# Performance work log

Hardware: AMD Instinct MI355X
Metric: run time of the kernel (lower is better)

## Reference

```python
import jax, jax.numpy as jnp
import numpy as np

INPUT_SIZE = 1024
HIDDEN_SIZE = 1024
N_LAYERS = 2
OUTPUT_SIZE = 4096
BATCH = 4096


def setup_inputs() -> dict:
    key = jax.random.key(0)
    ks = jax.random.split(key, 12)
    s = 1.0 / np.sqrt(HIDDEN_SIZE)
    u = lambda k, shp: jax.random.uniform(k, shp, jnp.float32, -s, s)
    return {
        "input": jax.random.normal(ks[0], (1, BATCH, INPUT_SIZE), jnp.float32),
        "hidden": jax.random.normal(ks[1], (N_LAYERS, BATCH, HIDDEN_SIZE), jnp.float32),
        # nn.RNN layer 0 params
        "W_ih0": u(ks[2], (HIDDEN_SIZE, INPUT_SIZE)),
        "W_hh0": u(ks[3], (HIDDEN_SIZE, HIDDEN_SIZE)),
        "b_ih0": u(ks[4], (HIDDEN_SIZE,)),
        "b_hh0": u(ks[5], (HIDDEN_SIZE,)),
        # nn.RNN layer 1 params (input is layer-0 hidden)
        "W_ih1": u(ks[6], (HIDDEN_SIZE, HIDDEN_SIZE)),
        "W_hh1": u(ks[7], (HIDDEN_SIZE, HIDDEN_SIZE)),
        "b_ih1": u(ks[8], (HIDDEN_SIZE,)),
        "b_hh1": u(ks[9], (HIDDEN_SIZE,)),
        # i2o Linear(input_size + hidden_size, output_size)
        "W_out": u(ks[10], (OUTPUT_SIZE, INPUT_SIZE + HIDDEN_SIZE)),
        "b_out": u(ks[11], (OUTPUT_SIZE,)),
    }


def reference(input, hidden, W_ih0, W_hh0, b_ih0, b_hh0,
              W_ih1, W_hh1, b_ih1, b_hh1, W_out, b_out):
    x = input[0]  # [B, input_size] (seq_len == 1)
    # nn.RNN single step, tanh nonlinearity, 2 layers
    h0 = jnp.tanh(x @ W_ih0.T + b_ih0 + hidden[0] @ W_hh0.T + b_hh0)   # [B, H]
    h1 = jnp.tanh(h0 @ W_ih1.T + b_ih1 + hidden[1] @ W_hh1.T + b_hh1)  # [B, H]
    new_hidden = jnp.stack([h0, h1], axis=0)  # [n_layers, B, H]
    # combined = cat(input[0], hidden[0]) where hidden is the NEW hidden
    combined = jnp.concatenate([x, h0], axis=1)  # [B, input+hidden]
    logits = combined @ W_out.T + b_out          # [B, output_size]
    out = jax.nn.log_softmax(logits, axis=1)
    return (out, new_hidden)
```

## Files before the change

kernel.cpp:

```cpp
#include <hip/hip_runtime.h>
#include <math.h>


typedef __attribute__((ext_vector_type(8))) short bf16x8;
typedef __attribute__((ext_vector_type(4))) float f32x4;

__device__ __forceinline__ unsigned short f2b_rne(float f) {
    unsigned int x = __float_as_uint(f);
    x += 0x7FFF + ((x >> 16) & 1);
    return (unsigned short)(x >> 16);
}

__device__ __forceinline__ void gload_lds16(const void* g, void* l) {
    __builtin_amdgcn_global_load_lds(
        (const __attribute__((address_space(1))) void*)g,
        (__attribute__((address_space(3))) void*)l,
        16, 0, 0);
}

struct CvtSeg { const float* src; unsigned short* dst; unsigned n8; };
struct CvtArgs { CvtSeg seg[7]; };

__global__ __launch_bounds__(256) void f2b_multi(CvtArgs a)
{
    unsigned i = blockIdx.x * 256 + threadIdx.x;
#pragma unroll
    for (int s = 0; s < 7; ++s) {
        if (i < a.seg[s].n8) {
            const float4* src = (const float4*)a.seg[s].src;
            float4 u = src[2 * (size_t)i];
            float4 v = src[2 * (size_t)i + 1];
            unsigned short t[8] = {
                f2b_rne(u.x), f2b_rne(u.y), f2b_rne(u.z), f2b_rne(u.w),
                f2b_rne(v.x), f2b_rne(v.y), f2b_rne(v.z), f2b_rne(v.w)};
            *(uint4*)(a.seg[s].dst + 8 * (size_t)i) = *(const uint4*)t;
            return;
        }
        i -= a.seg[s].n8;
    }
}

struct GemmP {
    const unsigned short *Aa, *Ab; int lda;
    const unsigned short *Wa, *Wb; int ldw;
    const float *ba, *bb;
    float* C; int ldc;
    unsigned short* Cb; int ldcb;
    int nx, nb, do_tanh;
};

template<int BM, int BN>
__device__ __forceinline__ void gemm2p_body(
    const GemmP& p, int bid0, unsigned short* As, unsigned short* Ws, int tid)
{
    constexpr int FM = BM / 32;
    constexpr int FN = BN / 32;
    int bid = (bid0 & 7) * (p.nb >> 3) + (bid0 >> 3);
    const int row0 = (bid / p.nx) * BM;
    const int col0 = (bid % p.nx) * BN;

    const int wid = tid >> 6, lane = tid & 63;
    const int wr = wid >> 1, wc = wid & 1;
    const int fr = lane & 15, fk = lane >> 4;

    f32x4 acc[FM][FN] = {};

    for (int h = 0; h < 2; ++h) {
        const unsigned short* A = h ? p.Ab : p.Aa;
        const unsigned short* W = h ? p.Wb : p.Wa;
        for (int k0 = 0; k0 < 1024; k0 += 32) {
#pragma unroll
            for (int i = 0; i < BM / 64; ++i) {
                int c = i * 256 + wid * 64 + lane;
                int r = c >> 2, ol = c & 3;
                int os = ol ^ ((r >> 1) & 3);
                gload_lds16(A + (size_t)(row0 + r) * p.lda + k0 + os * 8,
                            As + (i * 256 + wid * 64) * 8);
            }
#pragma unroll
            for (int i = 0; i < BN / 64; ++i) {
                int c = i * 256 + wid * 64 + lane;
                int r = c >> 2, ol = c & 3;
                int os = ol ^ ((r >> 1) & 3);
                gload_lds16(W + (size_t)(col0 + r) * p.ldw + k0 + os * 8,
                            Ws + (i * 256 + wid * 64) * 8);
            }
            __syncthreads();

            bf16x8 af[FM], wf[FN];
#pragma unroll
            for (int m = 0; m < FM; ++m) {
                int r = wr * (BM / 2) + m * 16 + fr;
                af[m] = *(const bf16x8*)&As[r * 32 + ((fk ^ ((r >> 1) & 3)) * 8)];
            }
#pragma unroll
            for (int n = 0; n < FN; ++n) {
                int r = wc * (BN / 2) + n * 16 + fr;
                wf[n] = *(const bf16x8*)&Ws[r * 32 + ((fk ^ ((r >> 1) & 3)) * 8)];
            }
#pragma unroll
            for (int m = 0; m < FM; ++m)
#pragma unroll
                for (int n = 0; n < FN; ++n)
                    acc[m][n] = __builtin_amdgcn_mfma_f32_16x16x32_bf16(
                        af[m], wf[n], acc[m][n], 0, 0, 0);
            __syncthreads();
        }
    }

    const bool dot = p.do_tanh != 0;
#pragma unroll
    for (int n = 0; n < FN; ++n) {
        const int col = col0 + wc * (BN / 2) + n * 16 + fr;
        float b = p.ba[col];
        if (p.bb) b += p.bb[col];
#pragma unroll
        for (int m = 0; m < FM; ++m) {
#pragma unroll
            for (int j = 0; j < 4; ++j) {
                const int r = row0 + wr * (BM / 2) + m * 16 + fk * 4 + j;
                float v = acc[m][n][j] + b;
                if (dot) v = tanhf(v);
                p.C[(size_t)r * p.ldc + col] = v;
                if (p.Cb) p.Cb[(size_t)r * p.ldcb + col] = f2b_rne(v);
            }
        }
    }
}

__global__ __launch_bounds__(256) void gemm1_k(GemmP p)
{
    __shared__ __align__(16) unsigned short As[128 * 32];
    __shared__ __align__(16) unsigned short Ws[64 * 32];
    gemm2p_body<128, 64>(p, blockIdx.x, As, Ws, threadIdx.x);
}

__device__ __forceinline__ void logsoftmax_row(float* __restrict__ p, int tid)
{
    const int lane = tid & 63;
    const int wv = tid >> 6;
    __shared__ float redm[4];
    __shared__ float reds[4];

    float v[16];
#pragma unroll
    for (int i = 0; i < 16; ++i) v[i] = p[tid + i * 256];

    float m = v[0];
#pragma unroll
    for (int i = 1; i < 16; ++i) m = fmaxf(m, v[i]);
#pragma unroll
    for (int off = 32; off; off >>= 1) m = fmaxf(m, __shfl_xor(m, off));
    if (lane == 0) redm[wv] = m;
    __syncthreads();
    m = fmaxf(fmaxf(redm[0], redm[1]), fmaxf(redm[2], redm[3]));

    float s = 0.f;
#pragma unroll
    for (int i = 0; i < 16; ++i) s += expf(v[i] - m);
#pragma unroll
    for (int off = 32; off; off >>= 1) s += __shfl_xor(s, off);
    if (lane == 0) reds[wv] = s;
    __syncthreads();
    s = reds[0] + reds[1] + reds[2] + reds[3];

    const float lse = m + logf(s);
#pragma unroll
    for (int i = 0; i < 16; ++i) p[tid + i * 256] = v[i] - lse;
}

__global__ __launch_bounds__(256) void g2sm_k(GemmP p, float* __restrict__ logits)
{
    if (blockIdx.x < 256) {
        __shared__ __align__(16) unsigned short As[128 * 32];
        __shared__ __align__(16) unsigned short Ws[128 * 32];
        gemm2p_body<128, 128>(p, blockIdx.x, As, Ws, threadIdx.x);
    } else {
        logsoftmax_row(logits + (size_t)(blockIdx.x - 256) * 4096, threadIdx.x);
    }
}


__device__ __forceinline__ void stage_half8(
    const unsigned short* __restrict__ src, int ld, int base_rc, int tau, int h,
    unsigned short* lds, int wid, int lane, bool isA)
{
    unsigned short* dst = lds + (tau & 1) * 16384 + h * 8192 + wid * 1024;
    const int k0 = (tau & 15) << 6;
#pragma unroll
    for (int i = 0; i < 2; ++i) {
        int c = wid * 128 + i * 64 + lane;
        int ir = c >> 3, cc = c & 7;
        int grow = isA ? (base_rc + h * 64 + (ir & 63) + ((ir >> 6) << 7))
                       : (base_rc + h * 32 + (ir & 31) + ((ir >> 5) << 6));
        int gk = k0 + (((cc ^ ir) & 7) << 3);
        gload_lds16(src + (size_t)grow * ld + gk, dst + i * 512);
    }
}

__global__ __launch_bounds__(512, 2) void gemm8p(
    const unsigned short* __restrict__ Aa, const unsigned short* __restrict__ Ab,
    const unsigned short* __restrict__ Wa, const unsigned short* __restrict__ Wb,
    int lda, int ldw, const float* __restrict__ bias,
    float* __restrict__ C, int ldc, int nx)
{
    constexpr int NT = 32;
    __shared__ __align__(16) unsigned short As[2 * 2 * 128 * 64];
    __shared__ __align__(16) unsigned short Bs[2 * 2 * 128 * 64];

    int bid = blockIdx.x;
    bid = (bid & 7) * 32 + (bid >> 3);
    const int row0 = (bid / nx) * 256;
    const int col0 = (bid % nx) * 256;

    const int tid = threadIdx.x;
    const int wid = tid >> 6, lane = tid & 63;
    const int wr = wid >> 2, wc = wid & 3;
    const int fr = lane & 15, fk = lane >> 4;
    const int ch0 = fk ^ (fr & 7);
    const int ch1 = ch0 ^ 4;

#define STA8(tau, h) stage_half8(((tau) < 16 ? Aa : Ab), lda, row0, (tau), (h), As, wid, lane, true)
#define STB8(tau, h) stage_half8(((tau) < 16 ? Wa : Wb), ldw, col0, (tau), (h), Bs, wid, lane, false)

    f32x4 acc[2][2][4][2] = {};

    STA8(0, 0); STB8(0, 0); STA8(0, 1); STB8(0, 1); STB8(1, 0); STA8(1, 0);
    asm volatile("s_waitcnt vmcnt(4)" ::: "memory");
    __builtin_amdgcn_s_barrier();

#define PHASE8(QM, QN, ...)                                                   \
    {                                                                         \
        const unsigned short* Ap_ = As + buf * 16384 + (QM) * 8192;           \
        const unsigned short* Bp_ = Bs + buf * 16384 + (QN) * 8192;           \
        bf16x8 af[4][2], wf[2][2];                                            \
        _Pragma("unroll") for (int mf = 0; mf < 4; ++mf) {                    \
            int ia = wr * 64 + mf * 16 + fr;                                  \
            af[mf][0] = *(const bf16x8*)&Ap_[ia * 64 + ch0 * 8];              \
            af[mf][1] = *(const bf16x8*)&Ap_[ia * 64 + ch1 * 8];              \
        }                                                                     \
        _Pragma("unroll") for (int nf = 0; nf < 2; ++nf) {                    \
            int ib = wc * 32 + nf * 16 + fr;                                  \
            wf[nf][0] = *(const bf16x8*)&Bp_[ib * 64 + ch0 * 8];              \
            wf[nf][1] = *(const bf16x8*)&Bp_[ib * 64 + ch1 * 8];              \
        }                                                                     \
        __VA_ARGS__                                                           \
        __builtin_amdgcn_s_barrier();                                         \
        asm volatile("s_waitcnt lgkmcnt(0)" ::: "memory");                    \
        __builtin_amdgcn_s_setprio(1);                                        \
        _Pragma("unroll") for (int mf = 0; mf < 4; ++mf)                      \
            _Pragma("unroll") for (int nf = 0; nf < 2; ++nf) {                \
                acc[QM][QN][mf][nf] = __builtin_amdgcn_mfma_f32_16x16x32_bf16(\
                    af[mf][0], wf[nf][0], acc[QM][QN][mf][nf], 0, 0, 0);      \
                acc[QM][QN][mf][nf] = __builtin_amdgcn_mfma_f32_16x16x32_bf16(\
                    af[mf][1], wf[nf][1], acc[QM][QN][mf][nf], 0, 0, 0);      \
            }                                                                 \
        __builtin_amdgcn_s_setprio(0);                                        \
    }

    for (int t = 0; t < NT; ++t) {
        const int buf = t & 1;
        PHASE8(0, 0, { if (t + 1 < NT) { STA8(t + 1, 1); STB8(t + 1, 1); } })
        __builtin_amdgcn_s_barrier();
        PHASE8(1, 0, {})
        __builtin_amdgcn_s_barrier();
        PHASE8(0, 1, { if (t + 2 < NT) STB8(t + 2, 0); })
        __builtin_amdgcn_s_barrier();
        PHASE8(1, 1, { if (t + 2 < NT) STA8(t + 2, 0); })
        if (t < NT - 1) {
            if (t <= NT - 3) asm volatile("s_waitcnt vmcnt(4)" ::: "memory");
            else             asm volatile("s_waitcnt vmcnt(0)" ::: "memory");
        }
        __builtin_amdgcn_s_barrier();
    }
#undef PHASE8
#undef STA8
#undef STB8

#pragma unroll
    for (int qm = 0; qm < 2; ++qm)
#pragma unroll
        for (int qn = 0; qn < 2; ++qn)
#pragma unroll
            for (int nf = 0; nf < 2; ++nf) {
                const int col = col0 + wc * 64 + qn * 32 + nf * 16 + fr;
                const float bv = bias[col];
#pragma unroll
                for (int mf = 0; mf < 4; ++mf) {
                    const int rowb = row0 + wr * 128 + qm * 64 + mf * 16 + fk * 4;
#pragma unroll
                    for (int j = 0; j < 4; ++j)
                        C[(size_t)(rowb + j) * ldc + col] =
                            acc[qm][qn][mf][nf][j] + bv;
                }
            }
}

extern "C" void kernel_launch(void* const* d_in, const int* in_sizes, int n_in,
                              void* d_out, int out_size, void* d_ws, size_t ws_size,
                              hipStream_t stream)
{
    (void)in_sizes; (void)n_in; (void)out_size; (void)ws_size;

    const float* input  = (const float*)d_in[0];
    const float* hidden = (const float*)d_in[1];
    const float* b_ih0  = (const float*)d_in[4];
    const float* b_hh0  = (const float*)d_in[5];
    const float* b_ih1  = (const float*)d_in[8];
    const float* b_hh1  = (const float*)d_in[9];
    const float* b_out  = (const float*)d_in[11];

    float* out = (float*)d_out;
    float* h0  = out + (size_t)4096 * 4096;
    float* h1  = h0 + (size_t)4096 * 1024;

    unsigned short* xb    = (unsigned short*)d_ws;
    unsigned short* hidb  = xb    + (size_t)4096 * 1024;
    unsigned short* h0b   = hidb  + (size_t)2 * 4096 * 1024;
    unsigned short* Wih0b = h0b   + (size_t)4096 * 1024;
    unsigned short* Whh0b = Wih0b + (size_t)1024 * 1024;
    unsigned short* Wih1b = Whh0b + (size_t)1024 * 1024;
    unsigned short* Whh1b = Wih1b + (size_t)1024 * 1024;
    unsigned short* Woutb = Whh1b + (size_t)1024 * 1024;
    unsigned short* hid0b = hidb;
    unsigned short* hid1b = hidb + (size_t)4096 * 1024;

    CvtArgs ca;
    ca.seg[0] = { input,                 xb,    4096u * 1024 / 8 };
    ca.seg[1] = { hidden,                hidb,  2u * 4096 * 1024 / 8 };
    ca.seg[2] = { (const float*)d_in[2], Wih0b, 1024u * 1024 / 8 };
    ca.seg[3] = { (const float*)d_in[3], Whh0b, 1024u * 1024 / 8 };
    ca.seg[4] = { (const float*)d_in[6], Wih1b, 1024u * 1024 / 8 };
    ca.seg[5] = { (const float*)d_in[7], Whh1b, 1024u * 1024 / 8 };
    ca.seg[6] = { (const float*)d_in[10],Woutb, 4096u * 2048 / 8 };
    hipLaunchKernelGGL(f2b_multi, dim3(12288), dim3(256), 0, stream, ca);

    GemmP p1;
    p1.Aa = xb;    p1.Ab = hid0b; p1.lda = 1024;
    p1.Wa = Wih0b; p1.Wb = Whh0b; p1.ldw = 1024;
    p1.ba = b_ih0; p1.bb = b_hh0;
    p1.C = h0; p1.ldc = 1024; p1.Cb = h0b; p1.ldcb = 1024;
    p1.nx = 16; p1.nb = 512; p1.do_tanh = 1;
    hipLaunchKernelGGL(gemm1_k, dim3(512), dim3(256), 0, stream, p1);

    hipLaunchKernelGGL(gemm8p, dim3(256), dim3(512), 0, stream,
                       xb, h0b, Woutb, Woutb + 1024, 1024, 2048,
                       b_out, out, 4096, 16);

    GemmP p2;
    p2.Aa = h0b;   p2.Ab = hid1b; p2.lda = 1024;
    p2.Wa = Wih1b; p2.Wb = Whh1b; p2.ldw = 1024;
    p2.ba = b_ih1; p2.bb = b_hh1;
    p2.C = h1; p2.ldc = 1024; p2.Cb = nullptr; p2.ldcb = 0;
    p2.nx = 8; p2.nb = 256; p2.do_tanh = 1;
    hipLaunchKernelGGL(g2sm_k, dim3(4352), dim3(256), 0, stream, p2, out);
}
```

Measured before the change: 200.3 us.

## Overlap weight conversion with first GEMM, restage gemm8p loop, coalesce epilogue via LDS

The fp32-to-bf16 conversion is split so only the tensors needed by the first GEMM are converted up front. The rest (hidden[1], layer-1 weights, W_out) are converted by extra blocks launched alongside the layer-0 GEMM, so conversion bandwidth overlaps with that GEMM's compute. The big output GEMM's inner loop is reordered to reuse A/B fragments across quadrant phases and to issue fewer LDS reads. Its epilogue now goes through shared memory to write coalesced float4 rows. The costs are more complex scheduling and barriers and an extra LDS round trip in the epilogue.

```diff
diff --git a/kernel.cpp b/kernel.cpp
--- a/kernel.cpp
+++ b/kernel.cpp
@@ -19,13 +19,12 @@
 }
 
 struct CvtSeg { const float* src; unsigned short* dst; unsigned n8; };
-struct CvtArgs { CvtSeg seg[7]; };
-
-__global__ __launch_bounds__(256) void f2b_multi(CvtArgs a)
-{
-    unsigned i = blockIdx.x * 256 + threadIdx.x;
-#pragma unroll
-    for (int s = 0; s < 7; ++s) {
+struct CvtArgs { CvtSeg seg[4]; };
+
+__device__ __forceinline__ void cvt_do(const CvtArgs& a, unsigned i)
+{
+#pragma unroll
+    for (int s = 0; s < 4; ++s) {
         if (i < a.seg[s].n8) {
             const float4* src = (const float4*)a.seg[s].src;
             float4 u = src[2 * (size_t)i];
@@ -40,6 +39,11 @@
     }
 }
 
+__global__ __launch_bounds__(256) void f2b_multi(CvtArgs a)
+{
+    cvt_do(a, blockIdx.x * 256u + threadIdx.x);
+}
+
 struct GemmP {
     const unsigned short *Aa, *Ab; int lda;
     const unsigned short *Wa, *Wb; int ldw;
@@ -128,11 +132,15 @@
     }
 }
 
-__global__ __launch_bounds__(256) void gemm1_k(GemmP p)
-{
-    __shared__ __align__(16) unsigned short As[128 * 32];
-    __shared__ __align__(16) unsigned short Ws[64 * 32];
-    gemm2p_body<128, 64>(p, blockIdx.x, As, Ws, threadIdx.x);
+__global__ __launch_bounds__(256) void g1cvt_k(GemmP p, CvtArgs ca)
+{
+    if (blockIdx.x < 512) {
+        __shared__ __align__(16) unsigned short As[128 * 32];
+        __shared__ __align__(16) unsigned short Ws[64 * 32];
+        gemm2p_body<128, 64>(p, blockIdx.x, As, Ws, threadIdx.x);
+    } else {
+        cvt_do(ca, (blockIdx.x - 512) * 256u + threadIdx.x);
+    }
 }
 
 __device__ __forceinline__ void logsoftmax_row(float* __restrict__ p, int tid)
@@ -205,8 +213,9 @@
     float* __restrict__ C, int ldc, int nx)
 {
     constexpr int NT = 32;
-    __shared__ __align__(16) unsigned short As[2 * 2 * 128 * 64];
-    __shared__ __align__(16) unsigned short Bs[2 * 2 * 128 * 64];
+    __shared__ __align__(16) unsigned short smem[65536];
+    unsigned short* As = smem;
+    unsigned short* Bs = smem + 32768;
 
     int bid = blockIdx.x;
     bid = (bid & 7) * 32 + (bid >> 3);
@@ -223,77 +232,103 @@
 #define STA8(tau, h) stage_half8(((tau) < 16 ? Aa : Ab), lda, row0, (tau), (h), As, wid, lane, true)
 #define STB8(tau, h) stage_half8(((tau) < 16 ? Wa : Wb), ldw, col0, (tau), (h), Bs, wid, lane, false)
 
+#define LDA(QM) { const unsigned short* Ap_ = Abase + (QM) * 8192;            \
+    _Pragma("unroll") for (int mf = 0; mf < 4; ++mf) {                        \
+        int ia = wr * 64 + mf * 16 + fr;                                      \
+        af[mf][0] = *(const bf16x8*)&Ap_[ia * 64 + ch0 * 8];                  \
+        af[mf][1] = *(const bf16x8*)&Ap_[ia * 64 + ch1 * 8]; } }
+
+#define LDB(QN) { const unsigned short* Bp_ = Bbase + (QN) * 8192;            \
+    _Pragma("unroll") for (int nf = 0; nf < 2; ++nf) {                        \
+        int ib = wc * 32 + nf * 16 + fr;                                      \
+        wf[nf][0] = *(const bf16x8*)&Bp_[ib * 64 + ch0 * 8];                  \
+        wf[nf][1] = *(const bf16x8*)&Bp_[ib * 64 + ch1 * 8]; } }
+
+#define MM(QM, QN, ...) {                                                     \
+    __builtin_amdgcn_s_barrier();                                             \
+    asm volatile("s_waitcnt lgkmcnt(0)" ::: "memory");                        \
+    __builtin_amdgcn_s_setprio(1);                                            \
+    _Pragma("unroll") for (int mf = 0; mf < 4; ++mf)                          \
+    _Pragma("unroll") for (int nf = 0; nf < 2; ++nf) {                        \
+        acc[QM][QN][mf][nf] = __builtin_amdgcn_mfma_f32_16x16x32_bf16(        \
+            af[mf][0], wf[nf][0], acc[QM][QN][mf][nf], 0, 0, 0);              \
+        acc[QM][QN][mf][nf] = __builtin_amdgcn_mfma_f32_16x16x32_bf16(        \
+            af[mf][1], wf[nf][1], acc[QM][QN][mf][nf], 0, 0, 0); }            \
+    __builtin_amdgcn_s_setprio(0);                                            \
+    __VA_ARGS__                                                               \
+    __builtin_amdgcn_s_barrier(); }
+
     f32x4 acc[2][2][4][2] = {};
-
-    STA8(0, 0); STB8(0, 0); STA8(0, 1); STB8(0, 1); STB8(1, 0); STA8(1, 0);
+    bf16x8 af[4][2], wf[2][2];
+
+    STA8(0, 0); STB8(0, 1);
+    STA8(0, 1); STB8(0, 0);
+    STA8(1, 0); STB8(1, 1);
     asm volatile("s_waitcnt vmcnt(4)" ::: "memory");
     __builtin_amdgcn_s_barrier();
 
-#define PHASE8(QM, QN, ...)                                                   \
-    {                                                                         \
-        const unsigned short* Ap_ = As + buf * 16384 + (QM) * 8192;           \
-        const unsigned short* Bp_ = Bs + buf * 16384 + (QN) * 8192;           \
-        bf16x8 af[4][2], wf[2][2];                                            \
-        _Pragma("unroll") for (int mf = 0; mf < 4; ++mf) {                    \
-            int ia = wr * 64 + mf * 16 + fr;                                  \
-            af[mf][0] = *(const bf16x8*)&Ap_[ia * 64 + ch0 * 8];              \
-            af[mf][1] = *(const bf16x8*)&Ap_[ia * 64 + ch1 * 8];              \
-        }                                                                     \
-        _Pragma("unroll") for (int nf = 0; nf < 2; ++nf) {                    \
-            int ib = wc * 32 + nf * 16 + fr;                                  \
-            wf[nf][0] = *(const bf16x8*)&Bp_[ib * 64 + ch0 * 8];              \
-            wf[nf][1] = *(const bf16x8*)&Bp_[ib * 64 + ch1 * 8];              \
-        }                                                                     \
-        __VA_ARGS__                                                           \
-        __builtin_amdgcn_s_barrier();                                         \
-        asm volatile("s_waitcnt lgkmcnt(0)" ::: "memory");                    \
-        __builtin_amdgcn_s_setprio(1);                                        \
-        _Pragma("unroll") for (int mf = 0; mf < 4; ++mf)                      \
-            _Pragma("unroll") for (int nf = 0; nf < 2; ++nf) {                \
-                acc[QM][QN][mf][nf] = __builtin_amdgcn_mfma_f32_16x16x32_bf16(\
-                    af[mf][0], wf[nf][0], acc[QM][QN][mf][nf], 0, 0, 0);      \
-                acc[QM][QN][mf][nf] = __builtin_amdgcn_mfma_f32_16x16x32_bf16(\
-                    af[mf][1], wf[nf][1], acc[QM][QN][mf][nf], 0, 0, 0);      \
-            }                                                                 \
-        __builtin_amdgcn_s_setprio(0);                                        \
-    }
-
     for (int t = 0; t < NT; ++t) {
-        const int buf = t & 1;
-        PHASE8(0, 0, { if (t + 1 < NT) { STA8(t + 1, 1); STB8(t + 1, 1); } })
-        __builtin_amdgcn_s_barrier();
-        PHASE8(1, 0, {})
-        __builtin_amdgcn_s_barrier();
-        PHASE8(0, 1, { if (t + 2 < NT) STB8(t + 2, 0); })
-        __builtin_amdgcn_s_barrier();
-        PHASE8(1, 1, { if (t + 2 < NT) STA8(t + 2, 0); })
-        if (t < NT - 1) {
-            if (t <= NT - 3) asm volatile("s_waitcnt vmcnt(4)" ::: "memory");
-            else             asm volatile("s_waitcnt vmcnt(0)" ::: "memory");
-        }
-        __builtin_amdgcn_s_barrier();
-    }
-#undef PHASE8
+        const unsigned short* Abase = As + (t & 1) * 16384;
+        const unsigned short* Bbase = Bs + (t & 1) * 16384;
+
+        LDA(0); LDB(0);
+        if (t + 1 < NT) { STA8(t + 1, 1); STB8(t + 1, 0); }
+        MM(0, 0, )
+        LDB(1);
+        MM(0, 1, )
+        LDA(1);
+        if (t + 2 < NT) STA8(t + 2, 0);
+        MM(1, 1, )
+        LDB(0);
+        if (t + 2 < NT) STB8(t + 2, 1);
+        if (t + 2 < NT) {
+            MM(1, 0, asm volatile("s_waitcnt vmcnt(4)" ::: "memory");)
+        } else if (t + 1 < NT) {
+            MM(1, 0, asm volatile("s_waitcnt vmcnt(0)" ::: "memory");)
+        } else {
+            MM(1, 0, )
+        }
+    }
+#undef MM
+#undef LDA
+#undef LDB
 #undef STA8
 #undef STB8
 
-#pragma unroll
-    for (int qm = 0; qm < 2; ++qm)
+    float bv[2][2];
+#pragma unroll
+    for (int qn = 0; qn < 2; ++qn)
+#pragma unroll
+        for (int nf = 0; nf < 2; ++nf)
+            bv[qn][nf] = bias[col0 + wc * 64 + qn * 32 + nf * 16 + fr];
+
+    float* Ct = (float*)smem;
+#pragma unroll
+    for (int qm = 0; qm < 2; ++qm) {
+        __syncthreads();
 #pragma unroll
         for (int qn = 0; qn < 2; ++qn)
 #pragma unroll
             for (int nf = 0; nf < 2; ++nf) {
-                const int col = col0 + wc * 64 + qn * 32 + nf * 16 + fr;
-                const float bv = bias[col];
-#pragma unroll
-                for (int mf = 0; mf < 4; ++mf) {
-                    const int rowb = row0 + wr * 128 + qm * 64 + mf * 16 + fk * 4;
-#pragma unroll
-                    for (int j = 0; j < 4; ++j)
-                        C[(size_t)(rowb + j) * ldc + col] =
-                            acc[qm][qn][mf][nf][j] + bv;
-                }
-            }
+                const int col = wc * 64 + qn * 32 + nf * 16 + fr;
+#pragma unroll
+                for (int mf = 0; mf < 4; ++mf)
+#pragma unroll
+                    for (int j = 0; j < 4; ++j) {
+                        int lr = wr * 64 + mf * 16 + fk * 4 + j;
+                        Ct[lr * 256 + col] = acc[qm][qn][mf][nf][j] + bv[qn][nf];
+                    }
+            }
+        __syncthreads();
+#pragma unroll
+        for (int k = 0; k < 16; ++k) {
+            int idx = k * 512 + tid;
+            int lrow = idx >> 6, c4 = idx & 63;
+            int grow = row0 + qm * 64 + (lrow & 63) + ((lrow >> 6) << 7);
+            *(float4*)&C[(size_t)grow * ldc + col0 + c4 * 4] =
+                *(const float4*)&Ct[lrow * 256 + c4 * 4];
+        }
+    }
 }
 
 extern "C" void kernel_launch(void* const* d_in, const int* in_sizes, int n_in,
@@ -325,15 +360,12 @@
     unsigned short* hid0b = hidb;
     unsigned short* hid1b = hidb + (size_t)4096 * 1024;
 
-    CvtArgs ca;
-    ca.seg[0] = { input,                 xb,    4096u * 1024 / 8 };
-    ca.seg[1] = { hidden,                hidb,  2u * 4096 * 1024 / 8 };
-    ca.seg[2] = { (const float*)d_in[2], Wih0b, 1024u * 1024 / 8 };
-    ca.seg[3] = { (const float*)d_in[3], Whh0b, 1024u * 1024 / 8 };
-    ca.seg[4] = { (const float*)d_in[6], Wih1b, 1024u * 1024 / 8 };
-    ca.seg[5] = { (const float*)d_in[7], Whh1b, 1024u * 1024 / 8 };
-    ca.seg[6] = { (const float*)d_in[10],Woutb, 4096u * 2048 / 8 };
-    hipLaunchKernelGGL(f2b_multi, dim3(12288), dim3(256), 0, stream, ca);
+    CvtArgs ca1;
+    ca1.seg[0] = { input,                 xb,    524288u };
+    ca1.seg[1] = { hidden,                hidb,  524288u };
+    ca1.seg[2] = { (const float*)d_in[2], Wih0b, 131072u };
+    ca1.seg[3] = { (const float*)d_in[3], Whh0b, 131072u };
+    hipLaunchKernelGGL(f2b_multi, dim3(5120), dim3(256), 0, stream, ca1);
 
     GemmP p1;
     p1.Aa = xb;    p1.Ab = hid0b; p1.lda = 1024;
@@ -341,7 +373,12 @@
     p1.ba = b_ih0; p1.bb = b_hh0;
     p1.C = h0; p1.ldc = 1024; p1.Cb = h0b; p1.ldcb = 1024;
     p1.nx = 16; p1.nb = 512; p1.do_tanh = 1;
-    hipLaunchKernelGGL(gemm1_k, dim3(512), dim3(256), 0, stream, p1);
+    CvtArgs ca2;
+    ca2.seg[0] = { hidden + (size_t)4096 * 1024, hid1b, 524288u };
+    ca2.seg[1] = { (const float*)d_in[6],  Wih1b, 131072u };
+    ca2.seg[2] = { (const float*)d_in[7],  Whh1b, 131072u };
+    ca2.seg[3] = { (const float*)d_in[10], Woutb, 1048576u };
+    hipLaunchKernelGGL(g1cvt_k, dim3(7680), dim3(256), 0, stream, p1, ca2);
 
     hipLaunchKernelGGL(gemm8p, dim3(256), dim3(512), 0, stream,
                        xb, h0b, Woutb, Woutb + 1024, 1024, 2048,
```

Result: slower. 244.6 us (+22.1%).
